# Optimization experiments

Hardware: AMD Instinct MI355X
Metric: run time of the kernel (lower is better)

## Reference

```python
import jax, jax.numpy as jnp
import numpy as np

NUM_USERS = 30000
NUM_ITEMS = 30000
N = NUM_USERS + NUM_ITEMS          # total graph nodes (users + items)
E = 800000                          # number of edges
EMBED_K = 64
INTENTS = 4
D = EMBED_K // INTENTS              # per-intent channel chunk
N_LAYERS = 1
ROUTING_ITERS = 2


def setup_inputs() -> dict:
    key = jax.random.key(0)
    k1, k2, k3, k4 = jax.random.split(key, 4)
    Gu = jax.random.normal(k1, (NUM_USERS, EMBED_K), jnp.float32) * 0.1
    Gi = jax.random.normal(k2, (NUM_ITEMS, EMBED_K), jnp.float32) * 0.1
    # head list: guarantee every node appears at least once as a head so that
    # D = 1/sqrt(row_degree) is finite (real CF graphs have no isolated rows)
    edge_h = jnp.concatenate([jnp.arange(N, dtype=jnp.int64),
                              jax.random.randint(k3, (E - N,), 0, N, dtype=jnp.int64)])
    edge_t = jax.random.randint(k4, (E,), 0, N, dtype=jnp.int64)
    return {"Gu": Gu, "Gi": Gi, "edge_h": edge_h, "edge_t": edge_t}


def _l2norm(x, eps=1e-12):
    # matches torch.nn.functional.normalize(dim=-1)
    return x / jnp.sqrt(jnp.maximum(jnp.sum(x * x, axis=-1, keepdims=True), eps))


def reference(Gu, Gi, edge_h, edge_t):
    ego = jnp.concatenate([Gu, Gi], axis=0)            # [N, K]
    all_emb = [ego]
    # routing attention logits per intent per edge (initialized to ones)
    A_values = jnp.ones((INTENTS, E), dtype=Gu.dtype)
    for _ in range(N_LAYERS):
        # split embed dim into INTENTS contiguous chunks -> [I, N, D]
        X = ego.reshape(N, INTENTS, D).transpose(1, 0, 2)
        Z = X
        for _t in range(ROUTING_ITERS):
            # softmax over intents per edge (pick=False path; p_train is always False)
            scores = jax.nn.softmax(A_values, axis=0)                    # [I, E]
            # per-intent row degrees (sparse.sum over dim=1 indexes rows = heads)
            deg = jnp.zeros((INTENTS, N), scores.dtype).at[:, edge_h].add(scores)
            d_col = 1.0 / jnp.sqrt(deg)                                  # [I, N]
            # D_col @ X, A @ (.), D_col @ (.)  -- note original applies D_col twice (as written)
            Y = d_col[..., None] * X                                     # [I, N, D]
            msg = scores[..., None] * Y[:, edge_t, :]                    # [I, E, D]
            Z = jnp.zeros((INTENTS, N, D), X.dtype).at[:, edge_h, :].add(msg)
            Z = d_col[..., None] * Z                                     # [I, N, D]
            # attention update: normalize(head) . tanh(normalize(tail))
            head = _l2norm(Z[:, edge_h, :])                              # [I, E, D]
            tail = _l2norm(X[:, edge_t, :])                              # [I, E, D]
            A_values = A_values + jnp.sum(head * jnp.tanh(tail), axis=-1)
        # concat intent chunks back along channel dim
        ego = Z.transpose(1, 0, 2).reshape(N, EMBED_K)
        all_emb.append(ego)
    out = jnp.mean(jnp.stack(all_emb, axis=1), axis=1)   # [N, K]
    return out[:NUM_USERS], out[NUM_USERS:]
```

## Files before the change

kernel.cpp:

```cpp
#include <hip/hip_runtime.h>
#include <hip/hip_fp16.h>


#define NUSERS 30000
#define NN     60000
#define EE     800000
#define SL     ((size_t)NN * 16)
#define SCAN_B ((NN + 255) / 256)
#define EV_B   ((EE / 4 + 255) / 256)
#define NW1_B  ((NN + 1 + 3) / 4)
#define OUTG   ((NN + 31) / 32)
#define OUT_B  ((((OUTG + 1) / 2) * 8))

__device__ __forceinline__ float getX(const float* __restrict__ Gu,
                                      const float* __restrict__ Gi,
                                      int n, int c) {
    return (n < NUSERS) ? Gu[n * 64 + c] : Gi[(n - NUSERS) * 64 + c];
}

__device__ __forceinline__ int clampN(int n) {
    return ((unsigned)n < (unsigned)NN) ? n : 0;
}

__device__ __forceinline__ __half2 bch2(float f) {
    return __builtin_bit_cast(__half2, f);
}


__global__ void edge_count(const int* __restrict__ eh, int* __restrict__ deg0,
                           int* __restrict__ rank) {
    int e4 = (blockIdx.x * blockDim.x + threadIdx.x) * 4;
    if (e4 >= EE) return;
    int4 h = *(const int4*)(eh + e4);
    int4 r;
    r.x = atomicAdd(&deg0[clampN(h.x)], 1);
    r.y = atomicAdd(&deg0[clampN(h.y)], 1);
    r.z = atomicAdd(&deg0[clampN(h.z)], 1);
    r.w = atomicAdd(&deg0[clampN(h.w)], 1);
    *(int4*)(rank + e4) = r;
}

__global__ void scan_local(const int* __restrict__ deg0, int* __restrict__ offsets,
                           int* __restrict__ bsum) {
    int gid = blockIdx.x * 256 + threadIdx.x;
    int lane = threadIdx.x & 63, w = threadIdx.x >> 6;
    int vdeg = (gid < NN) ? deg0[gid] : 0;
    int x = vdeg;
    #pragma unroll
    for (int d = 1; d < 64; d <<= 1) {
        int y = __shfl_up(x, d, 64);
        if (lane >= d) x += y;
    }
    __shared__ int wsum[4];
    if (lane == 63) wsum[w] = x;
    __syncthreads();
    int wpre = 0;
    #pragma unroll
    for (int j = 0; j < 4; ++j) wpre += (j < w) ? wsum[j] : 0;
    int incl = x + wpre;
    if (gid < NN) offsets[gid] = incl - vdeg;
    if (threadIdx.x == 255) bsum[blockIdx.x] = incl;
}

__global__ void scan_add2(int* __restrict__ offsets, const int* __restrict__ bsum) {
    int tid = threadIdx.x, lane = tid & 63, w = tid >> 6;
    int vv = (tid < SCAN_B) ? bsum[tid] : 0;
    int x = vv;
    #pragma unroll
    for (int d = 1; d < 64; d <<= 1) {
        int y = __shfl_up(x, d, 64);
        if (lane >= d) x += y;
    }
    __shared__ int wsum[4];
    __shared__ int bpre;
    if (lane == 63) wsum[w] = x;
    __syncthreads();
    int wpre = 0;
    #pragma unroll
    for (int j = 0; j < 4; ++j) wpre += (j < w) ? wsum[j] : 0;
    if (tid == blockIdx.x) bpre = x + wpre - vv;
    __syncthreads();
    int gid = blockIdx.x * 256 + tid;
    if (gid < NN) offsets[gid] += bpre;
    if (gid == 0) offsets[NN] = EE;
}

__global__ void scatter_prep(const int* __restrict__ eh, const int* __restrict__ et,
                             const int* __restrict__ rank,
                             const int* __restrict__ offsets,
                             int2* __restrict__ csr_ht,
                             const float* __restrict__ Gu, const float* __restrict__ Gi,
                             const int* __restrict__ deg0,
                             __half* __restrict__ Ytab, __half* __restrict__ Ttab) {
    if (blockIdx.x < EV_B) {
        int e4 = (blockIdx.x * 256 + threadIdx.x) * 4;
        if (e4 >= EE) return;
        int4 h = *(const int4*)(eh + e4);
        int4 t = *(const int4*)(et + e4);
        int4 r = *(const int4*)(rank + e4);
        int h0 = clampN(h.x), h1 = clampN(h.y), h2 = clampN(h.z), h3 = clampN(h.w);
        int s0 = offsets[h0] + r.x;
        if ((unsigned)s0 < EE) csr_ht[s0] = make_int2(h0, clampN(t.x));
        int s1 = offsets[h1] + r.y;
        if ((unsigned)s1 < EE) csr_ht[s1] = make_int2(h1, clampN(t.y));
        int s2 = offsets[h2] + r.z;
        if ((unsigned)s2 < EE) csr_ht[s2] = make_int2(h2, clampN(t.z));
        int s3 = offsets[h3] + r.w;
        if ((unsigned)s3 < EE) csr_ht[s3] = make_int2(h3, clampN(t.w));
    } else {
        int n = (blockIdx.x - EV_B) * 4 + (threadIdx.x >> 6);
        if (n > NN) return;
        int lane = threadIdx.x & 63;
        float x = (n < NN) ? getX(Gu, Gi, n, lane) : 0.f;
        float sx = x * x;
        #pragma unroll
        for (int m = 1; m < 16; m <<= 1) sx += __shfl_xor(sx, m, 64);
        float invx = rsqrtf(fmaxf(sx, 1e-12f));
        float d0 = rsqrtf(fmaxf(0.25f * (float)((n < NN) ? deg0[n] : 1), 1e-30f));
        size_t a = (size_t)n * 64 + lane;
        Ytab[a] = __float2half(d0 * x);
        Ttab[a] = __float2half(tanhf(x * invx));
    }
}

__global__ void zacc(const int* __restrict__ offsets, const int2* __restrict__ csr_ht,
                     const __half* __restrict__ Ytab, __half* __restrict__ ZN) {
    int n = blockIdx.x * 4 + (threadIdx.x >> 6);
    if (n >= NN) return;
    int lane = threadIdx.x & 63;
    int e2 = lane >> 5, cc = lane & 31;
    int s0 = offsets[n], s1 = offsets[n + 1];
    float accx = 0.f, accy = 0.f;
    for (int base = s0; base < s1; base += 2) {
        int kk = base + e2;
        bool act = kk < s1;
        int kc = (kk < EE) ? kk : (EE - 1);
        int t = act ? csr_ht[kc].y : NN;
        __half2 y = *(const __half2*)(Ytab + (size_t)t * 64 + cc * 2);
        float2 yf = __half22float2(y);
        accx += yf.x; accy += yf.y;
    }
    accx += __shfl_xor(accx, 32, 64);
    accy += __shfl_xor(accy, 32, 64);
    float ss = accx * accx + accy * accy;
    ss += __shfl_xor(ss, 1, 64);
    ss += __shfl_xor(ss, 2, 64);
    ss += __shfl_xor(ss, 4, 64);
    float inv = rsqrtf(fmaxf(ss, 1e-12f));
    if (lane < 32) {
        *(__half2*)(ZN + (size_t)n * 64 + cc * 2) =
            __floats2half2_rn(accx * inv, accy * inv);
    }
}

__global__ void attdot(const int2* __restrict__ csr_ht,
                       const __half* __restrict__ ZN, const __half* __restrict__ Ttab,
                       __half* __restrict__ v4) {
    int k = blockIdx.x * 256 + threadIdx.x;
    if (k >= EE) return;
    int2 ht = csr_ht[k];
    int h = ht.x, t = ht.y;
    const float4* zp = (const float4*)(ZN + (size_t)h * 64);
    const float4* tp = (const float4*)(Ttab + (size_t)t * 64);
    float dot[4];
    #pragma unroll
    for (int i = 0; i < 4; ++i) {
        float4 za = zp[2 * i], zb = zp[2 * i + 1];
        float4 ta = tp[2 * i], tb = tp[2 * i + 1];
        __half2 acc = __floats2half2_rn(0.f, 0.f);
        acc = __hfma2(bch2(za.x), bch2(ta.x), acc);
        acc = __hfma2(bch2(za.y), bch2(ta.y), acc);
        acc = __hfma2(bch2(za.z), bch2(ta.z), acc);
        acc = __hfma2(bch2(za.w), bch2(ta.w), acc);
        acc = __hfma2(bch2(zb.x), bch2(tb.x), acc);
        acc = __hfma2(bch2(zb.y), bch2(tb.y), acc);
        acc = __hfma2(bch2(zb.z), bch2(tb.z), acc);
        acc = __hfma2(bch2(zb.w), bch2(tb.w), acc);
        float2 f = __half22float2(acc);
        dot[i] = f.x + f.y;
    }
    __half2 o01 = __floats2half2_rn(dot[0], dot[1]);
    __half2 o23 = __floats2half2_rn(dot[2], dot[3]);
    int2 st;
    st.x = __builtin_bit_cast(int, o01);
    st.y = __builtin_bit_cast(int, o23);
    *(int2*)(v4 + (size_t)k * 4) = st;
}

__global__ void sm_dcol_y1(const int* __restrict__ offsets, const __half* __restrict__ v4,
                           __half* __restrict__ scores, float* __restrict__ dcol1,
                           const float* __restrict__ Gu, const float* __restrict__ Gi,
                           __half* __restrict__ Y1s) {
    int n = blockIdx.x * 4 + (threadIdx.x >> 6);
    if (n >= NN) return;
    int lane = threadIdx.x & 63;
    int s0 = offsets[n], s1 = offsets[n + 1];
    float sum0 = 0.f, sum1 = 0.f, sum2 = 0.f, sum3 = 0.f;
    for (int k = s0 + lane; k < s1; k += 64) {
        int2 raw = *(const int2*)(v4 + (size_t)k * 4);
        __half2 p01 = __builtin_bit_cast(__half2, raw.x);
        __half2 p23 = __builtin_bit_cast(__half2, raw.y);
        float2 fa = __half22float2(p01), fb = __half22float2(p23);
        float v0 = fa.x, v1 = fa.y, v2 = fb.x, v3 = fb.y;
        float mx = fmaxf(fmaxf(v0, v1), fmaxf(v2, v3));
        float e0 = __expf(v0 - mx), e1 = __expf(v1 - mx);
        float e2 = __expf(v2 - mx), e3 = __expf(v3 - mx);
        float inv = 1.f / (e0 + e1 + e2 + e3);
        e0 *= inv; e1 *= inv; e2 *= inv; e3 *= inv;
        scores[k]          = __float2half(e0);
        scores[EE + k]     = __float2half(e1);
        scores[2 * EE + k] = __float2half(e2);
        scores[3 * EE + k] = __float2half(e3);
        sum0 += e0; sum1 += e1; sum2 += e2; sum3 += e3;
    }
    #pragma unroll
    for (int m = 1; m < 64; m <<= 1) {
        sum0 += __shfl_xor(sum0, m, 64);
        sum1 += __shfl_xor(sum1, m, 64);
        sum2 += __shfl_xor(sum2, m, 64);
        sum3 += __shfl_xor(sum3, m, 64);
    }
    int i = lane >> 4, ch = lane & 15;
    float dsel = (i == 0) ? sum0 : (i == 1) ? sum1 : (i == 2) ? sum2 : sum3;
    float d = rsqrtf(fmaxf(dsel, 1e-30f));
    if (lane < 4) {
        float ds = (lane == 0) ? sum0 : (lane == 1) ? sum1 : (lane == 2) ? sum2 : sum3;
        dcol1[n * 4 + lane] = rsqrtf(fmaxf(ds, 1e-30f));
    }
    float x = getX(Gu, Gi, n, lane);
    Y1s[(size_t)i * SL + (size_t)n * 16 + ch] = __float2half(d * x);
}

__global__ void outk(const int* __restrict__ offsets, const int2* __restrict__ csr_ht,
                     const __half* __restrict__ Y1s, const __half* __restrict__ scores,
                     const float* __restrict__ dcol1,
                     const float* __restrict__ Gu, const float* __restrict__ Gi,
                     float* __restrict__ out) {
    int b = blockIdx.x, tid = threadIdx.x;
    int xcd = b & 7;
    int i = xcd >> 1;
    int g = (b >> 3) * 2 + (xcd & 1);
    if (g >= OUTG) return;
    int lane = tid & 63;
    int c = lane & 7;
    int n = g * 32 + (tid >> 6) * 8 + (lane >> 3);
    if (n >= NN) return;
    int s0 = offsets[n], s1 = offsets[n + 1];
    int deg = s1 - s0;
    int md = deg;
    md = max(md, __shfl_xor(md, 8, 64));
    md = max(md, __shfl_xor(md, 16, 64));
    md = max(md, __shfl_xor(md, 32, 64));
    const __half* Yi = Y1s + (size_t)i * SL;
    const __half* si = scores + (size_t)i * EE;
    float accx = 0.f, accy = 0.f;
    for (int j = 0; j < md; j += 8) {
        int base = s0 + j;
        #pragma unroll
        for (int u = 0; u < 8; ++u) {
            int kk = base + u;
            bool act = kk < s1;
            int kc = act ? kk : s0;
            int t = csr_ht[kc].y;
            float s = act ? __half2float(si[kc]) : 0.f;
            __half2 y = *(const __half2*)(Yi + (size_t)t * 16 + c * 2);
            float2 yf = __half22float2(y);
            accx = fmaf(s, yf.x, accx);
            accy = fmaf(s, yf.y, accy);
        }
    }
    float d = dcol1[n * 4 + i];
    int ch = i * 16 + c * 2;
    const float* xr = (n < NUSERS) ? (Gu + n * 64 + ch) : (Gi + (n - NUSERS) * 64 + ch);
    float2 x2 = *(const float2*)xr;
    float2 o;
    o.x = 0.5f * (x2.x + d * accx);
    o.y = 0.5f * (x2.y + d * accy);
    *(float2*)(out + (size_t)n * 64 + ch) = o;
}


extern "C" void kernel_launch(void* const* d_in, const int* in_sizes, int n_in,
                              void* d_out, int out_size, void* d_ws, size_t ws_size,
                              hipStream_t stream) {
    const float* Gu = (const float*)d_in[0];
    const float* Gi = (const float*)d_in[1];
    const int* eh = (const int*)d_in[2];
    const int* et = (const int*)d_in[3];
    float* out = (float*)d_out;

    char* p = (char*)d_ws;
    __half* v4       = (__half*)p;     p += (size_t)EE * 4 * 2;
    __half* scores   = (__half*)p;     p += (size_t)EE * 4 * 2;
    int2*   csr_ht   = (int2*)p;       p += (size_t)EE * 8;
    int*    rank     = (int*)p;        p += (size_t)EE * 4;
    int*    offsets  = (int*)p;        p += ((size_t)(NN + 1) * 4 + 15) / 16 * 16;
    int*    deg0     = (int*)p;        p += (size_t)NN * 4;
    int*    bsum     = (int*)p;        p += ((size_t)SCAN_B * 4 + 15) / 16 * 16;
    float*  dcol1    = (float*)p;      p += (size_t)NN * 4 * 4;
    __half* Ytab     = (__half*)p;     p += (size_t)(NN + 1) * 64 * 2;
    __half* Ttab     = (__half*)p;     p += (size_t)(NN + 1) * 64 * 2;
    __half* ZN       = (__half*)p;
    __half* Y1s      = Ytab;

    const int nw_blocks = (NN + 3) / 4;

    hipMemsetAsync(deg0, 0, NN * sizeof(int), stream);
    edge_count<<<EV_B, 256, 0, stream>>>(eh, deg0, rank);
    scan_local<<<SCAN_B, 256, 0, stream>>>(deg0, offsets, bsum);
    scan_add2<<<SCAN_B, 256, 0, stream>>>(offsets, bsum);

    scatter_prep<<<EV_B + NW1_B, 256, 0, stream>>>(eh, et, rank, offsets, csr_ht,
                                                   Gu, Gi, deg0, Ytab, Ttab);

    zacc<<<nw_blocks, 256, 0, stream>>>(offsets, csr_ht, Ytab, ZN);
    attdot<<<(EE + 255) / 256, 256, 0, stream>>>(csr_ht, ZN, Ttab, v4);

    sm_dcol_y1<<<nw_blocks, 256, 0, stream>>>(offsets, v4, scores, dcol1, Gu, Gi, Y1s);

    outk<<<OUT_B, 256, 0, stream>>>(offsets, csr_ht, Y1s, scores, dcol1, Gu, Gi, out);
}
```

Measured before the change: 281.3 us.

## Switch scores and Y1 to node-interleaved layout; one 32-lane group per node

The softmax scores are now stored interleaved per edge (4 halves in one int2) instead of intent-major planes. Y1 is stored as a node-major [N,64] row instead of per-intent planes. The output gather kernel now processes all four intents of a node with one 32-lane group, so each edge's tail index and scores are fetched once rather than once per intent. zacc is likewise changed to one half-wave per node with a 4-way unrolled edge loop. The trade-off is that the XCD-aware per-intent partitioning is dropped, and each gathered row becomes 128 bytes instead of 32, which may hurt L2 locality.

```diff
diff --git a/kernel.cpp b/kernel.cpp
--- a/kernel.cpp
+++ b/kernel.cpp
@@ -5,12 +5,10 @@
 #define NUSERS 30000
 #define NN     60000
 #define EE     800000
-#define SL     ((size_t)NN * 16)
 #define SCAN_B ((NN + 255) / 256)
 #define EV_B   ((EE / 4 + 255) / 256)
 #define NW1_B  ((NN + 1 + 3) / 4)
-#define OUTG   ((NN + 31) / 32)
-#define OUT_B  ((((OUTG + 1) / 2) * 8))
+#define N8_B   ((NN + 7) / 8)
 
 __device__ __forceinline__ float getX(const float* __restrict__ Gu,
                                       const float* __restrict__ Gi,
@@ -125,32 +123,31 @@
 
 __global__ void zacc(const int* __restrict__ offsets, const int2* __restrict__ csr_ht,
                      const __half* __restrict__ Ytab, __half* __restrict__ ZN) {
-    int n = blockIdx.x * 4 + (threadIdx.x >> 6);
+    int tid = threadIdx.x;
+    int n = blockIdx.x * 8 + (tid >> 5);
     if (n >= NN) return;
-    int lane = threadIdx.x & 63;
-    int e2 = lane >> 5, cc = lane & 31;
+    int cc = tid & 31;
     int s0 = offsets[n], s1 = offsets[n + 1];
     float accx = 0.f, accy = 0.f;
-    for (int base = s0; base < s1; base += 2) {
-        int kk = base + e2;
-        bool act = kk < s1;
-        int kc = (kk < EE) ? kk : (EE - 1);
-        int t = act ? csr_ht[kc].y : NN;
-        __half2 y = *(const __half2*)(Ytab + (size_t)t * 64 + cc * 2);
-        float2 yf = __half22float2(y);
-        accx += yf.x; accy += yf.y;
-    }
-    accx += __shfl_xor(accx, 32, 64);
-    accy += __shfl_xor(accy, 32, 64);
+    for (int base = s0; base < s1; base += 4) {
+        #pragma unroll
+        for (int u = 0; u < 4; ++u) {
+            int kk = base + u;
+            bool act = kk < s1;
+            int kc = act ? kk : s0;
+            int t = act ? csr_ht[kc].y : NN;
+            __half2 y = *(const __half2*)(Ytab + (size_t)t * 64 + cc * 2);
+            float2 yf = __half22float2(y);
+            accx += yf.x; accy += yf.y;
+        }
+    }
     float ss = accx * accx + accy * accy;
     ss += __shfl_xor(ss, 1, 64);
     ss += __shfl_xor(ss, 2, 64);
     ss += __shfl_xor(ss, 4, 64);
     float inv = rsqrtf(fmaxf(ss, 1e-12f));
-    if (lane < 32) {
-        *(__half2*)(ZN + (size_t)n * 64 + cc * 2) =
-            __floats2half2_rn(accx * inv, accy * inv);
-    }
+    *(__half2*)(ZN + (size_t)n * 64 + cc * 2) =
+        __floats2half2_rn(accx * inv, accy * inv);
 }
 
 __global__ void attdot(const int2* __restrict__ csr_ht,
@@ -188,9 +185,9 @@
 }
 
 __global__ void sm_dcol_y1(const int* __restrict__ offsets, const __half* __restrict__ v4,
-                           __half* __restrict__ scores, float* __restrict__ dcol1,
+                           __half* __restrict__ s4, float* __restrict__ dcol1,
                            const float* __restrict__ Gu, const float* __restrict__ Gi,
-                           __half* __restrict__ Y1s) {
+                           __half* __restrict__ Y1i) {
     int n = blockIdx.x * 4 + (threadIdx.x >> 6);
     if (n >= NN) return;
     int lane = threadIdx.x & 63;
@@ -207,10 +204,12 @@
         float e2 = __expf(v2 - mx), e3 = __expf(v3 - mx);
         float inv = 1.f / (e0 + e1 + e2 + e3);
         e0 *= inv; e1 *= inv; e2 *= inv; e3 *= inv;
-        scores[k]          = __float2half(e0);
-        scores[EE + k]     = __float2half(e1);
-        scores[2 * EE + k] = __float2half(e2);
-        scores[3 * EE + k] = __float2half(e3);
+        __half2 q01 = __floats2half2_rn(e0, e1);
+        __half2 q23 = __floats2half2_rn(e2, e3);
+        int2 st;
+        st.x = __builtin_bit_cast(int, q01);
+        st.y = __builtin_bit_cast(int, q23);
+        *(int2*)(s4 + (size_t)k * 4) = st;
         sum0 += e0; sum1 += e1; sum2 += e2; sum3 += e3;
     }
     #pragma unroll
@@ -220,7 +219,7 @@
         sum2 += __shfl_xor(sum2, m, 64);
         sum3 += __shfl_xor(sum3, m, 64);
     }
-    int i = lane >> 4, ch = lane & 15;
+    int i = lane >> 4;
     float dsel = (i == 0) ? sum0 : (i == 1) ? sum1 : (i == 2) ? sum2 : sum3;
     float d = rsqrtf(fmaxf(dsel, 1e-30f));
     if (lane < 4) {
@@ -228,50 +227,41 @@
         dcol1[n * 4 + lane] = rsqrtf(fmaxf(ds, 1e-30f));
     }
     float x = getX(Gu, Gi, n, lane);
-    Y1s[(size_t)i * SL + (size_t)n * 16 + ch] = __float2half(d * x);
+    Y1i[(size_t)n * 64 + lane] = __float2half(d * x);
 }
 
 __global__ void outk(const int* __restrict__ offsets, const int2* __restrict__ csr_ht,
-                     const __half* __restrict__ Y1s, const __half* __restrict__ scores,
+                     const __half* __restrict__ Y1i, const __half* __restrict__ s4,
                      const float* __restrict__ dcol1,
                      const float* __restrict__ Gu, const float* __restrict__ Gi,
                      float* __restrict__ out) {
-    int b = blockIdx.x, tid = threadIdx.x;
-    int xcd = b & 7;
-    int i = xcd >> 1;
-    int g = (b >> 3) * 2 + (xcd & 1);
-    if (g >= OUTG) return;
-    int lane = tid & 63;
-    int c = lane & 7;
-    int n = g * 32 + (tid >> 6) * 8 + (lane >> 3);
+    int tid = threadIdx.x;
+    int n = blockIdx.x * 8 + (tid >> 5);
     if (n >= NN) return;
+    int cc = tid & 31;
     int s0 = offsets[n], s1 = offsets[n + 1];
-    int deg = s1 - s0;
-    int md = deg;
-    md = max(md, __shfl_xor(md, 8, 64));
-    md = max(md, __shfl_xor(md, 16, 64));
-    md = max(md, __shfl_xor(md, 32, 64));
-    const __half* Yi = Y1s + (size_t)i * SL;
-    const __half* si = scores + (size_t)i * EE;
     float accx = 0.f, accy = 0.f;
-    for (int j = 0; j < md; j += 8) {
-        int base = s0 + j;
+    for (int base = s0; base < s1; base += 4) {
         #pragma unroll
-        for (int u = 0; u < 8; ++u) {
+        for (int u = 0; u < 4; ++u) {
             int kk = base + u;
             bool act = kk < s1;
             int kc = act ? kk : s0;
             int t = csr_ht[kc].y;
-            float s = act ? __half2float(si[kc]) : 0.f;
-            __half2 y = *(const __half2*)(Yi + (size_t)t * 16 + c * 2);
+            int2 raw = *(const int2*)(s4 + (size_t)kc * 4);
+            int word = (cc & 16) ? raw.y : raw.x;
+            unsigned short us = (unsigned short)(word >> ((cc & 8) ? 16 : 0));
+            float s = act ? __half2float(__builtin_bit_cast(__half, us)) : 0.f;
+            __half2 y = *(const __half2*)(Y1i + (size_t)t * 64 + cc * 2);
             float2 yf = __half22float2(y);
             accx = fmaf(s, yf.x, accx);
             accy = fmaf(s, yf.y, accy);
         }
     }
-    float d = dcol1[n * 4 + i];
-    int ch = i * 16 + c * 2;
-    const float* xr = (n < NUSERS) ? (Gu + n * 64 + ch) : (Gi + (n - NUSERS) * 64 + ch);
+    float d = dcol1[n * 4 + (cc >> 3)];
+    int ch = cc * 2;
+    const float* xr = (n < NUSERS) ? (Gu + (size_t)n * 64 + ch)
+                                   : (Gi + (size_t)(n - NUSERS) * 64 + ch);
     float2 x2 = *(const float2*)xr;
     float2 o;
     o.x = 0.5f * (x2.x + d * accx);
@@ -291,7 +281,7 @@
 
     char* p = (char*)d_ws;
     __half* v4       = (__half*)p;     p += (size_t)EE * 4 * 2;
-    __half* scores   = (__half*)p;     p += (size_t)EE * 4 * 2;
+    __half* s4       = (__half*)p;     p += (size_t)EE * 4 * 2;
     int2*   csr_ht   = (int2*)p;       p += (size_t)EE * 8;
     int*    rank     = (int*)p;        p += (size_t)EE * 4;
     int*    offsets  = (int*)p;        p += ((size_t)(NN + 1) * 4 + 15) / 16 * 16;
@@ -301,7 +291,7 @@
     __half* Ytab     = (__half*)p;     p += (size_t)(NN + 1) * 64 * 2;
     __half* Ttab     = (__half*)p;     p += (size_t)(NN + 1) * 64 * 2;
     __half* ZN       = (__half*)p;
-    __half* Y1s      = Ytab;
+    __half* Y1i      = Ytab;
 
     const int nw_blocks = (NN + 3) / 4;
 
@@ -313,10 +303,10 @@
     scatter_prep<<<EV_B + NW1_B, 256, 0, stream>>>(eh, et, rank, offsets, csr_ht,
                                                    Gu, Gi, deg0, Ytab, Ttab);
 
-    zacc<<<nw_blocks, 256, 0, stream>>>(offsets, csr_ht, Ytab, ZN);
+    zacc<<<N8_B, 256, 0, stream>>>(offsets, csr_ht, Ytab, ZN);
     attdot<<<(EE + 255) / 256, 256, 0, stream>>>(csr_ht, ZN, Ttab, v4);
 
-    sm_dcol_y1<<<nw_blocks, 256, 0, stream>>>(offsets, v4, scores, dcol1, Gu, Gi, Y1s);
-
-    outk<<<OUT_B, 256, 0, stream>>>(offsets, csr_ht, Y1s, scores, dcol1, Gu, Gi, out);
-}
+    sm_dcol_y1<<<nw_blocks, 256, 0, stream>>>(offsets, v4, s4, dcol1, Gu, Gi, Y1i);
+
+    outk<<<N8_B, 256, 0, stream>>>(offsets, csr_ht, Y1i, s4, dcol1, Gu, Gi, out);
+}
```

After: 254.9 us. 1.1x faster.
